# Optimization experiments

Hardware: AMD Instinct MI355X
Metric: run time of the kernel (lower is better)

The kernel has to match this reference:

```python
import jax, jax.numpy as jnp
import numpy as np

N, E, D, H = 20000, 320000, 300, 2
NEG_SLOPE = 0.2  # PyG GATConv default LeakyReLU slope


def setup_inputs() -> dict:
    key = jax.random.key(0)
    ks = jax.random.split(key, 8)
    return {
        "x": jax.random.normal(ks[0], (N, D), dtype=jnp.float32),
        "edge_index": jax.random.randint(ks[1], (2, E), 0, N, dtype=jnp.int64),
        "W": jax.random.normal(ks[2], (D, H, D), dtype=jnp.float32) * 0.05,
        "att_src": jax.random.normal(ks[3], (H, D), dtype=jnp.float32) * 0.05,
        "att_dst": jax.random.normal(ks[4], (H, D), dtype=jnp.float32) * 0.05,
        "bias": jax.random.normal(ks[5], (D,), dtype=jnp.float32) * 0.05,
        "lin_w": jax.random.normal(ks[6], (D, 1), dtype=jnp.float32) * 0.05,
        "lin_b": jax.random.normal(ks[7], (1,), dtype=jnp.float32) * 0.05,
    }


def reference(x, edge_index, W, att_src, att_dst, bias, lin_w, lin_b):
    n = x.shape[0]
    # add self-loops (PyG GATConv default)
    loops = jnp.arange(n, dtype=edge_index.dtype)
    src = jnp.concatenate([edge_index[0], loops])  # [E+N]
    dst = jnp.concatenate([edge_index[1], loops])
    # per-head linear projection: [N, H, D]
    xp = jnp.einsum('nd,dhe->nhe', x, W)
    # per-node attention logits [N, H]
    a_src = jnp.sum(xp * att_src, axis=-1)
    a_dst = jnp.sum(xp * att_dst, axis=-1)
    # per-edge score, LeakyReLU, segment softmax over incoming edges of dst
    e = jax.nn.leaky_relu(a_src[src] + a_dst[dst], NEG_SLOPE)  # [Et, H]
    emax = jax.ops.segment_max(e, dst, num_segments=n)  # self-loops ensure non-empty
    ee = jnp.exp(e - emax[dst])
    denom = jax.ops.segment_sum(ee, dst, num_segments=n)
    alpha = ee / denom[dst]  # [Et, H]
    # weighted scatter-add aggregation
    msg = xp[src] * alpha[:, :, None]  # [Et, H, D]
    out = jax.ops.segment_sum(msg, dst, num_segments=n)  # [N, H, D]
    out = out.mean(axis=1) + bias  # concat=False -> head average, then bias
    out = jax.nn.relu(out)
    return out @ lin_w + lin_b  # [N, 1]
```

## Files before the change

### kernel.cpp

```cpp
#include <hip/hip_runtime.h>
#include <math.h>

#define Nn 20000
#define Ee 320000
#define Dd 300
#define Hh 2
#define Cc 600
#define KP 320
#define MP 20096
#define NP 640
#define SQ 640

typedef _Float16 f16;
typedef __attribute__((ext_vector_type(8))) _Float16 f16x8;
typedef __attribute__((ext_vector_type(4))) _Float16 f16x4;
typedef __attribute__((ext_vector_type(2))) _Float16 f16x2;
typedef __attribute__((ext_vector_type(4))) float f32x4;

__device__ __forceinline__ float lrelu(float x) { return x > 0.f ? x : 0.2f * x; }

__global__ __launch_bounds__(256) void k_cvtX(const float* __restrict__ x, f16* __restrict__ xh) {
  int idx = blockIdx.x * 256 + threadIdx.x;
  const int KQ = KP / 4;
  if (idx >= MP * KQ) return;
  int r = idx / KQ, k0 = (idx - r * KQ) * 4;
  float a0 = 0.f, a1 = 0.f, a2 = 0.f, a3 = 0.f;
  if (r < Nn && k0 < Dd) {
    float4 v = *(const float4*)(x + (size_t)r * Dd + k0);
    a0 = v.x; a1 = v.y; a2 = v.z; a3 = v.w;
  }
  f16x4 h;
  h[0] = (f16)a0; h[1] = (f16)a1; h[2] = (f16)a2; h[3] = (f16)a3;
  *(f16x4*)(xh + (size_t)r * KP + k0) = h;
}

__global__ __launch_bounds__(256) void k_cvtW(const float* __restrict__ W, f16* __restrict__ Wh) {
  int idx = blockIdx.x * 256 + threadIdx.x;
  const int KQ = KP / 4;
  if (idx >= NP * KQ) return;
  int c = idx % NP, k0 = (idx / NP) * 4;
  f16x4 h;
#pragma unroll
  for (int j = 0; j < 4; ++j) {
    int k = k0 + j;
    h[j] = (f16)((k < Dd && c < Cc) ? W[(size_t)k * Cc + c] : 0.f);
  }
  *(f16x4*)(Wh + (size_t)c * KP + k0) = h;
}

__global__ __launch_bounds__(256) void k_prep(const float* __restrict__ W,
                                              const float* __restrict__ att_src,
                                              const float* __restrict__ att_dst,
                                              float* __restrict__ vatt) {
  int wid = (blockIdx.x * 256 + threadIdx.x) >> 6;
  int ln = threadIdx.x & 63;
  if (wid >= Dd) return;
  float s0 = 0.f, s1 = 0.f, t0 = 0.f, t1 = 0.f;
  for (int e = ln; e < Dd; e += 64) {
    float w0 = W[(size_t)wid * Cc + e];
    float w1 = W[(size_t)wid * Cc + Dd + e];
    s0 += w0 * att_src[e];  s1 += w1 * att_src[Dd + e];
    t0 += w0 * att_dst[e];  t1 += w1 * att_dst[Dd + e];
  }
  for (int o = 32; o > 0; o >>= 1) {
    s0 += __shfl_down(s0, o, 64); s1 += __shfl_down(s1, o, 64);
    t0 += __shfl_down(t0, o, 64); t1 += __shfl_down(t1, o, 64);
  }
  if (ln == 0) {
    vatt[wid * 4 + 0] = s0; vatt[wid * 4 + 1] = s1;
    vatt[wid * 4 + 2] = t0; vatt[wid * 4 + 3] = t1;
  }
}

__global__ __launch_bounds__(256) void k_logits2(const float* __restrict__ x,
                                                 const float* __restrict__ vatt,
                                                 float* __restrict__ a_src,
                                                 float* __restrict__ a_dst) {
  int wid = (blockIdx.x * 256 + threadIdx.x) >> 6;
  int ln = threadIdx.x & 63;
  if (wid >= Nn) return;
  const float* xr = x + (size_t)wid * Dd;
  float s0 = 0.f, s1 = 0.f, t0 = 0.f, t1 = 0.f;
  for (int d = ln; d < Dd; d += 64) {
    float xv = xr[d];
    float4 vv = *(const float4*)(vatt + d * 4);
    s0 += xv * vv.x; s1 += xv * vv.y; t0 += xv * vv.z; t1 += xv * vv.w;
  }
  for (int o = 32; o > 0; o >>= 1) {
    s0 += __shfl_down(s0, o, 64); s1 += __shfl_down(s1, o, 64);
    t0 += __shfl_down(t0, o, 64); t1 += __shfl_down(t1, o, 64);
  }
  if (ln == 0) {
    a_src[wid * 2 + 0] = s0; a_src[wid * 2 + 1] = s1;
    a_dst[wid * 2 + 0] = t0; a_dst[wid * 2 + 1] = t1;
  }
}

__global__ __launch_bounds__(256) void k_mm(const f16* __restrict__ xh, const f16* __restrict__ Wh,
                                            f16* __restrict__ xq) {
  __shared__ __align__(16) f16 Ash[128][40];
  __shared__ __align__(16) f16 Bsh[64][40];
  int m0 = blockIdx.x * 128, n0 = blockIdx.y * 64;
  int tid = threadIdx.x, wv = tid >> 6, lane = tid & 63;
  int srow = tid >> 2, skq = (tid & 3) * 8;
  int akq = (lane >> 4) * 8;
  f32x4 acc[2][4] = {};
  for (int ks = 0; ks < KP / 32; ++ks) {
    f16x8 va0 = *(const f16x8*)(xh + (size_t)(m0 + srow) * KP + ks * 32 + skq);
    f16x8 va1 = *(const f16x8*)(xh + (size_t)(m0 + 64 + srow) * KP + ks * 32 + skq);
    f16x8 vb  = *(const f16x8*)(Wh + (size_t)(n0 + srow) * KP + ks * 32 + skq);
    __syncthreads();
    *(f16x8*)&Ash[srow][skq]      = va0;
    *(f16x8*)&Ash[64 + srow][skq] = va1;
    *(f16x8*)&Bsh[srow][skq]      = vb;
    __syncthreads();
    f16x8 fa0 = *(const f16x8*)&Ash[32 * wv + (lane & 15)][akq];
    f16x8 fa1 = *(const f16x8*)&Ash[32 * wv + 16 + (lane & 15)][akq];
#pragma unroll
    for (int nt = 0; nt < 4; ++nt) {
      f16x8 fb = *(const f16x8*)&Bsh[16 * nt + (lane & 15)][akq];
      acc[0][nt] = __builtin_amdgcn_mfma_f32_16x16x32_f16(fa0, fb, acc[0][nt], 0, 0, 0);
      acc[1][nt] = __builtin_amdgcn_mfma_f32_16x16x32_f16(fa1, fb, acc[1][nt], 0, 0, 0);
    }
  }
#pragma unroll
  for (int g = 0; g < 2; ++g) {
#pragma unroll
    for (int nt = 0; nt < 4; ++nt) {
      int col = n0 + 16 * nt + (lane & 15);
      if (col < Cc) {
        int rbase = m0 + 32 * wv + 16 * g + ((lane >> 4) * 4);
#pragma unroll
        for (int i = 0; i < 4; ++i) {
          int row = rbase + i;
          if (row < Nn) xq[(size_t)row * SQ + col] = (f16)acc[g][nt][i];
        }
      }
    }
  }
}

__global__ void k_hist(const int* __restrict__ ei, int* __restrict__ cnt) {
  int e = blockIdx.x * 256 + threadIdx.x;
  if (e < Ee) atomicAdd(&cnt[ei[Ee + e]], 1);
}

__global__ __launch_bounds__(1024) void k_scan(const int* __restrict__ cnt, int* __restrict__ offs) {
  __shared__ int wsum[16];
  __shared__ int carry_s;
  int tid = threadIdx.x, wv = tid >> 6, ln = tid & 63;
  if (tid == 0) carry_s = 0;
  __syncthreads();
  for (int base = 0; base < Nn; base += 1024) {
    int i = base + tid;
    int v = (i < Nn) ? cnt[i] : 0;
    int s = v;
    for (int o = 1; o < 64; o <<= 1) {
      int t = __shfl_up(s, o, 64);
      if (ln >= o) s += t;
    }
    if (ln == 63) wsum[wv] = s;
    __syncthreads();
    if (wv == 0) {
      int w = (ln < 16) ? wsum[ln] : 0;
      for (int o = 1; o < 16; o <<= 1) {
        int t = __shfl_up(w, o, 64);
        if (ln >= o) w += t;
      }
      if (ln < 16) wsum[ln] = w;
    }
    __syncthreads();
    int carry = carry_s;
    int excl = carry + (wv > 0 ? wsum[wv - 1] : 0) + s - v;
    if (i < Nn) offs[i] = excl;
    __syncthreads();
    if (tid == 1023) carry_s = carry + wsum[15];
    __syncthreads();
  }
  if (tid == 0) offs[Nn] = carry_s;
}

__global__ void k_scatter(const int* __restrict__ ei, const int* __restrict__ offs,
                          int* __restrict__ cur, int* __restrict__ srt) {
  int e = blockIdx.x * 256 + threadIdx.x;
  if (e < Ee) {
    int s = ei[e], d = ei[Ee + e];
    int pos = offs[d] + atomicAdd(&cur[d], 1);
    srt[pos] = s;
  }
}

__global__ __launch_bounds__(256) void k_agg(const f16* __restrict__ xq,
    const float* __restrict__ a_src, const float* __restrict__ a_dst,
    const int* __restrict__ offs, const int* __restrict__ srt,
    const float* __restrict__ bias, const float* __restrict__ lin_w,
    const float* __restrict__ lin_b, float* __restrict__ out) {
  __shared__ float sAgg[4][600];
  int tid = threadIdx.x, wv = tid >> 6, ln = tid & 63;
  int n = blockIdx.x * 4 + wv;
  int beg = offs[n], deg = offs[n + 1] - beg;
  float2 adv = *(const float2*)(a_dst + 2 * n);
  float2 asv = *(const float2*)(a_src + 2 * n);
  float se0 = lrelu(asv.x + adv.x), se1 = lrelu(asv.y + adv.y);

  float m0 = se0, m1 = se1, s0 = 0.f, s1 = 0.f;
  int ss = -1; float ee0 = 0.f, ee1 = 0.f;
  for (int base = 0; base < deg; base += 64) {
    if (ln < deg - base) {
      int s = srt[beg + base + ln];
      float2 av = *(const float2*)(a_src + 2 * s);
      ss = s; ee0 = lrelu(av.x + adv.x); ee1 = lrelu(av.y + adv.y);
      if (ee0 > m0) { s0 *= __expf(m0 - ee0); m0 = ee0; }
      s0 += __expf(ee0 - m0);
      if (ee1 > m1) { s1 *= __expf(m1 - ee1); m1 = ee1; }
      s1 += __expf(ee1 - m1);
    }
  }
  for (int o = 32; o > 0; o >>= 1) {
    float om = __shfl_xor(m0, o, 64), os = __shfl_xor(s0, o, 64);
    float nm = fmaxf(m0, om);
    s0 = s0 * __expf(m0 - nm) + os * __expf(om - nm); m0 = nm;
    om = __shfl_xor(m1, o, 64); os = __shfl_xor(s1, o, 64);
    nm = fmaxf(m1, om);
    s1 = s1 * __expf(m1 - nm) + os * __expf(om - nm); m1 = nm;
  }
  { float nm = fmaxf(m0, se0); s0 = s0 * __expf(m0 - nm) + __expf(se0 - nm); m0 = nm; }
  { float nm = fmaxf(m1, se1); s1 = s1 * __expf(m1 - nm) + __expf(se1 - nm); m1 = nm; }
  float inv0 = 1.f / s0, inv1 = 1.f / s1;

  float acc[10] = {};
  auto addrow = [&](const f16* row, float p0, float p1) {
#pragma unroll
    for (int k = 0; k < 5; ++k) {
      int c = 2 * ln + 128 * k;
      if (c < Cc) {
        f16x2 hv = *(const f16x2*)(row + c);
        float p = (c < Dd) ? p0 : p1;
        acc[2 * k]     += p * (float)hv[0];
        acc[2 * k + 1] += p * (float)hv[1];
      }
    }
  };

  if (deg <= 64) {
    float p0 = __expf(ee0 - m0) * inv0, p1 = __expf(ee1 - m1) * inv1;
    for (int j = 0; j < deg; ++j) {
      int s = __shfl(ss, j, 64);
      float q0 = __shfl(p0, j, 64), q1 = __shfl(p1, j, 64);
      addrow(xq + (size_t)s * SQ, q0, q1);
    }
  } else {
    for (int base = 0; base < deg; base += 64) {
      int cnt = min(64, deg - base);
      float p0 = 0.f, p1 = 0.f; int s2 = -1;
      if (ln < cnt) {
        int s = srt[beg + base + ln];
        float2 av = *(const float2*)(a_src + 2 * s);
        s2 = s;
        p0 = __expf(lrelu(av.x + adv.x) - m0) * inv0;
        p1 = __expf(lrelu(av.y + adv.y) - m1) * inv1;
      }
      for (int j = 0; j < cnt; ++j) {
        int s = __shfl(s2, j, 64);
        float q0 = __shfl(p0, j, 64), q1 = __shfl(p1, j, 64);
        addrow(xq + (size_t)s * SQ, q0, q1);
      }
    }
  }
  addrow(xq + (size_t)n * SQ, __expf(se0 - m0) * inv0, __expf(se1 - m1) * inv1);

#pragma unroll
  for (int k = 0; k < 5; ++k) {
    int c = 2 * ln + 128 * k;
    if (c < Cc) { sAgg[wv][c] = acc[2 * k]; sAgg[wv][c + 1] = acc[2 * k + 1]; }
  }
  __syncthreads();

  float part = 0.f;
#pragma unroll
  for (int k = 0; k < 5; ++k) {
    int d = ln + 64 * k;
    if (d < Dd) {
      float v = 0.5f * (sAgg[wv][d] + sAgg[wv][d + Dd]) + bias[d];
      v = fmaxf(v, 0.f);
      part += v * lin_w[d];
    }
  }
  for (int o = 32; o > 0; o >>= 1) part += __shfl_xor(part, o, 64);
  if (ln == 0) out[n] = part + lin_b[0];
}

extern "C" void kernel_launch(void* const* d_in, const int* in_sizes, int n_in,
                              void* d_out, int out_size, void* d_ws, size_t ws_size,
                              hipStream_t stream) {
  const float* x       = (const float*)d_in[0];
  const int*   ei      = (const int*)d_in[1];
  const float* W       = (const float*)d_in[2];
  const float* att_src = (const float*)d_in[3];
  const float* att_dst = (const float*)d_in[4];
  const float* bias    = (const float*)d_in[5];
  const float* lin_w   = (const float*)d_in[6];
  const float* lin_b   = (const float*)d_in[7];
  float* out = (float*)d_out;

  char* ws = (char*)d_ws;
  size_t off = 0;
  auto alloc = [&](size_t bytes) {
    void* p = ws + off;
    off = (off + bytes + 255) & ~(size_t)255;
    return p;
  };
  f16*   xq    = (f16*)alloc((size_t)Nn * SQ * 2);
  f16*   xh    = (f16*)alloc((size_t)MP * KP * 2);
  f16*   Wh    = (f16*)alloc((size_t)NP * KP * 2);
  float* vatt  = (float*)alloc((size_t)Dd * 4 * 4);
  float* a_src = (float*)alloc((size_t)Nn * Hh * 4);
  float* a_dst = (float*)alloc((size_t)Nn * Hh * 4);
  int*   cnt   = (int*)alloc((size_t)Nn * 4);
  int*   offs  = (int*)alloc((size_t)(Nn + 1) * 4);
  int*   cur   = (int*)alloc((size_t)Nn * 4);
  int*   srt   = (int*)alloc((size_t)Ee * 4);

  hipMemsetAsync(cnt, 0, (size_t)Nn * 4, stream);
  hipMemsetAsync(cur, 0, (size_t)Nn * 4, stream);

  k_cvtX<<<(MP * (KP / 4) + 255) / 256, 256, 0, stream>>>(x, xh);
  k_cvtW<<<(NP * (KP / 4) + 255) / 256, 256, 0, stream>>>(W, Wh);
  k_prep<<<(Dd * 64 + 255) / 256, 256, 0, stream>>>(W, att_src, att_dst, vatt);
  k_logits2<<<(Nn * 64 + 255) / 256, 256, 0, stream>>>(x, vatt, a_src, a_dst);
  k_mm<<<dim3(MP / 128, NP / 64), 256, 0, stream>>>(xh, Wh, xq);
  k_hist<<<(Ee + 255) / 256, 256, 0, stream>>>(ei, cnt);
  k_scan<<<1, 1024, 0, stream>>>(cnt, offs);
  k_scatter<<<(Ee + 255) / 256, 256, 0, stream>>>(ei, offs, cur, srt);
  k_agg<<<Nn / 4, 256, 0, stream>>>(xq, a_src, a_dst, offs, srt, bias, lin_w, lin_b, out);
}
```

Baseline: 243.7 us.

## Fuse preprocessing kernels, drop memsets, single-pass scan, widen aggregation loads

```diff
diff --git a/kernel.cpp b/kernel.cpp
--- a/kernel.cpp
+++ b/kernel.cpp
@@ -14,85 +14,80 @@
 typedef _Float16 f16;
 typedef __attribute__((ext_vector_type(8))) _Float16 f16x8;
 typedef __attribute__((ext_vector_type(4))) _Float16 f16x4;
-typedef __attribute__((ext_vector_type(2))) _Float16 f16x2;
 typedef __attribute__((ext_vector_type(4))) float f32x4;
 
 __device__ __forceinline__ float lrelu(float x) { return x > 0.f ? x : 0.2f * x; }
 
-__global__ __launch_bounds__(256) void k_cvtX(const float* __restrict__ x, f16* __restrict__ xh) {
-  int idx = blockIdx.x * 256 + threadIdx.x;
-  const int KQ = KP / 4;
-  if (idx >= MP * KQ) return;
-  int r = idx / KQ, k0 = (idx - r * KQ) * 4;
-  float a0 = 0.f, a1 = 0.f, a2 = 0.f, a3 = 0.f;
-  if (r < Nn && k0 < Dd) {
-    float4 v = *(const float4*)(x + (size_t)r * Dd + k0);
-    a0 = v.x; a1 = v.y; a2 = v.z; a3 = v.w;
-  }
-  f16x4 h;
-  h[0] = (f16)a0; h[1] = (f16)a1; h[2] = (f16)a2; h[3] = (f16)a3;
-  *(f16x4*)(xh + (size_t)r * KP + k0) = h;
-}
-
-__global__ __launch_bounds__(256) void k_cvtW(const float* __restrict__ W, f16* __restrict__ Wh) {
-  int idx = blockIdx.x * 256 + threadIdx.x;
-  const int KQ = KP / 4;
-  if (idx >= NP * KQ) return;
-  int c = idx % NP, k0 = (idx / NP) * 4;
-  f16x4 h;
-#pragma unroll
-  for (int j = 0; j < 4; ++j) {
-    int k = k0 + j;
-    h[j] = (f16)((k < Dd && c < Cc) ? W[(size_t)k * Cc + c] : 0.f);
-  }
-  *(f16x4*)(Wh + (size_t)c * KP + k0) = h;
-}
-
-__global__ __launch_bounds__(256) void k_prep(const float* __restrict__ W,
+__global__ __launch_bounds__(256) void k_pre2(const float* __restrict__ W,
                                               const float* __restrict__ att_src,
                                               const float* __restrict__ att_dst,
-                                              float* __restrict__ vatt) {
-  int wid = (blockIdx.x * 256 + threadIdx.x) >> 6;
-  int ln = threadIdx.x & 63;
-  if (wid >= Dd) return;
+                                              f16* __restrict__ Wh, float* __restrict__ vatt) {
+  int idx = blockIdx.x * 256 + threadIdx.x;
+  {
+    int c = idx % NP, k0 = (idx / NP) * 4;
+    f16x4 h;
+#pragma unroll
+    for (int j = 0; j < 4; ++j) {
+      int k = k0 + j;
+      h[j] = (f16)((k < Dd && c < Cc) ? W[(size_t)k * Cc + c] : 0.f);
+    }
+    *(f16x4*)(Wh + (size_t)c * KP + k0) = h;
+  }
+  int wid = idx >> 6, ln = idx & 63;
+  if (wid < Dd) {
+    float s0 = 0.f, s1 = 0.f, t0 = 0.f, t1 = 0.f;
+    for (int e = ln; e < Dd; e += 64) {
+      float w0 = W[(size_t)wid * Cc + e];
+      float w1 = W[(size_t)wid * Cc + Dd + e];
+      s0 += w0 * att_src[e];  s1 += w1 * att_src[Dd + e];
+      t0 += w0 * att_dst[e];  t1 += w1 * att_dst[Dd + e];
+    }
+    for (int o = 32; o > 0; o >>= 1) {
+      s0 += __shfl_down(s0, o, 64); s1 += __shfl_down(s1, o, 64);
+      t0 += __shfl_down(t0, o, 64); t1 += __shfl_down(t1, o, 64);
+    }
+    if (ln == 0) {
+      vatt[wid * 4 + 0] = s0; vatt[wid * 4 + 1] = s1;
+      vatt[wid * 4 + 2] = t0; vatt[wid * 4 + 3] = t1;
+    }
+  }
+}
+
+__global__ __launch_bounds__(256) void k_pre1(const float* __restrict__ x,
+                                              const float* __restrict__ vatt,
+                                              f16* __restrict__ xh,
+                                              float* __restrict__ a_src, float* __restrict__ a_dst,
+                                              int* __restrict__ cnt) {
+  int gid = blockIdx.x * 256 + threadIdx.x;
+  if (gid < Nn) cnt[gid] = 0;
+  int wv = threadIdx.x >> 6, ln = threadIdx.x & 63;
+  int n = blockIdx.x * 4 + wv;
+  if (n >= MP) return;
+  if (n >= Nn) {
+#pragma unroll
+    for (int k = 0; k < 5; ++k) xh[(size_t)n * KP + ln + 64 * k] = (f16)0.f;
+    return;
+  }
+  const float* xr = x + (size_t)n * Dd;
   float s0 = 0.f, s1 = 0.f, t0 = 0.f, t1 = 0.f;
-  for (int e = ln; e < Dd; e += 64) {
-    float w0 = W[(size_t)wid * Cc + e];
-    float w1 = W[(size_t)wid * Cc + Dd + e];
-    s0 += w0 * att_src[e];  s1 += w1 * att_src[Dd + e];
-    t0 += w0 * att_dst[e];  t1 += w1 * att_dst[Dd + e];
+#pragma unroll
+  for (int k = 0; k < 5; ++k) {
+    int d = ln + 64 * k;
+    float xv = 0.f;
+    if (d < Dd) {
+      xv = xr[d];
+      float4 vv = *(const float4*)(vatt + d * 4);
+      s0 += xv * vv.x; s1 += xv * vv.y; t0 += xv * vv.z; t1 += xv * vv.w;
+    }
+    xh[(size_t)n * KP + d] = (f16)xv;
   }
   for (int o = 32; o > 0; o >>= 1) {
     s0 += __shfl_down(s0, o, 64); s1 += __shfl_down(s1, o, 64);
     t0 += __shfl_down(t0, o, 64); t1 += __shfl_down(t1, o, 64);
   }
   if (ln == 0) {
-    vatt[wid * 4 + 0] = s0; vatt[wid * 4 + 1] = s1;
-    vatt[wid * 4 + 2] = t0; vatt[wid * 4 + 3] = t1;
-  }
-}
-
-__global__ __launch_bounds__(256) void k_logits2(const float* __restrict__ x,
-                                                 const float* __restrict__ vatt,
-                                                 float* __restrict__ a_src,
-                                                 float* __restrict__ a_dst) {
-  int wid = (blockIdx.x * 256 + threadIdx.x) >> 6;
-  int ln = threadIdx.x & 63;
-  if (wid >= Nn) return;
-  const float* xr = x + (size_t)wid * Dd;
-  float s0 = 0.f, s1 = 0.f, t0 = 0.f, t1 = 0.f;
-  for (int d = ln; d < Dd; d += 64) {
-    float xv = xr[d];
-    float4 vv = *(const float4*)(vatt + d * 4);
-    s0 += xv * vv.x; s1 += xv * vv.y; t0 += xv * vv.z; t1 += xv * vv.w;
-  }
-  for (int o = 32; o > 0; o >>= 1) {
-    s0 += __shfl_down(s0, o, 64); s1 += __shfl_down(s1, o, 64);
-    t0 += __shfl_down(t0, o, 64); t1 += __shfl_down(t1, o, 64);
-  }
-  if (ln == 0) {
-    a_src[wid * 2 + 0] = s0; a_src[wid * 2 + 1] = s1;
-    a_dst[wid * 2 + 0] = t0; a_dst[wid * 2 + 1] = t1;
+    a_src[n * 2 + 0] = s0; a_src[n * 2 + 1] = s1;
+    a_dst[n * 2 + 0] = t0; a_dst[n * 2 + 1] = t1;
   }
 }
 
@@ -145,47 +140,57 @@
   if (e < Ee) atomicAdd(&cnt[ei[Ee + e]], 1);
 }
 
-__global__ __launch_bounds__(1024) void k_scan(const int* __restrict__ cnt, int* __restrict__ offs) {
+__global__ __launch_bounds__(1024) void k_scan(const int* __restrict__ cnt,
+                                               int* __restrict__ offs, int* __restrict__ cur) {
   __shared__ int wsum[16];
-  __shared__ int carry_s;
-  int tid = threadIdx.x, wv = tid >> 6, ln = tid & 63;
-  if (tid == 0) carry_s = 0;
+  int t = threadIdx.x, wv = t >> 6, ln = t & 63;
+  int i0 = t * 20;
+  int v[20];
+  int tot = 0;
+  if (i0 < Nn) {
+    const int4* p = (const int4*)(cnt + i0);
+#pragma unroll
+    for (int q = 0; q < 5; ++q) {
+      int4 w = p[q];
+      v[4 * q] = w.x; v[4 * q + 1] = w.y; v[4 * q + 2] = w.z; v[4 * q + 3] = w.w;
+    }
+#pragma unroll
+    for (int j = 0; j < 20; ++j) tot += v[j];
+  }
+  int s = tot;
+  for (int o = 1; o < 64; o <<= 1) {
+    int u = __shfl_up(s, o, 64);
+    if (ln >= o) s += u;
+  }
+  if (ln == 63) wsum[wv] = s;
   __syncthreads();
-  for (int base = 0; base < Nn; base += 1024) {
-    int i = base + tid;
-    int v = (i < Nn) ? cnt[i] : 0;
-    int s = v;
-    for (int o = 1; o < 64; o <<= 1) {
-      int t = __shfl_up(s, o, 64);
-      if (ln >= o) s += t;
-    }
-    if (ln == 63) wsum[wv] = s;
-    __syncthreads();
-    if (wv == 0) {
-      int w = (ln < 16) ? wsum[ln] : 0;
-      for (int o = 1; o < 16; o <<= 1) {
-        int t = __shfl_up(w, o, 64);
-        if (ln >= o) w += t;
-      }
-      if (ln < 16) wsum[ln] = w;
-    }
-    __syncthreads();
-    int carry = carry_s;
-    int excl = carry + (wv > 0 ? wsum[wv - 1] : 0) + s - v;
-    if (i < Nn) offs[i] = excl;
-    __syncthreads();
-    if (tid == 1023) carry_s = carry + wsum[15];
-    __syncthreads();
-  }
-  if (tid == 0) offs[Nn] = carry_s;
-}
-
-__global__ void k_scatter(const int* __restrict__ ei, const int* __restrict__ offs,
-                          int* __restrict__ cur, int* __restrict__ srt) {
+  if (wv == 0) {
+    int w = (ln < 16) ? wsum[ln] : 0;
+    for (int o = 1; o < 16; o <<= 1) {
+      int u = __shfl_up(w, o, 64);
+      if (ln >= o) w += u;
+    }
+    if (ln < 16) wsum[ln] = w;
+  }
+  __syncthreads();
+  if (i0 < Nn) {
+    int run = (wv > 0 ? wsum[wv - 1] : 0) + (s - tot);
+#pragma unroll
+    for (int j = 0; j < 20; ++j) {
+      offs[i0 + j] = run;
+      cur[i0 + j] = run;
+      run += v[j];
+    }
+  }
+  if (t == 0) offs[Nn] = wsum[15];
+}
+
+__global__ void k_scatter(const int* __restrict__ ei, int* __restrict__ cur,
+                          int* __restrict__ srt) {
   int e = blockIdx.x * 256 + threadIdx.x;
   if (e < Ee) {
     int s = ei[e], d = ei[Ee + e];
-    int pos = offs[d] + atomicAdd(&cur[d], 1);
+    int pos = atomicAdd(&cur[d], 1);
     srt[pos] = s;
   }
 }
@@ -228,22 +233,25 @@
   { float nm = fmaxf(m1, se1); s1 = s1 * __expf(m1 - nm) + __expf(se1 - nm); m1 = nm; }
   float inv0 = 1.f / s0, inv1 = 1.f / s1;
 
-  float acc[10] = {};
+  float acc[12] = {};
   auto addrow = [&](const f16* row, float p0, float p1) {
 #pragma unroll
-    for (int k = 0; k < 5; ++k) {
-      int c = 2 * ln + 128 * k;
+    for (int k = 0; k < 3; ++k) {
+      int c = 4 * ln + 256 * k;
       if (c < Cc) {
-        f16x2 hv = *(const f16x2*)(row + c);
+        f16x4 hv = *(const f16x4*)(row + c);
         float p = (c < Dd) ? p0 : p1;
-        acc[2 * k]     += p * (float)hv[0];
-        acc[2 * k + 1] += p * (float)hv[1];
+        acc[4 * k + 0] += p * (float)hv[0];
+        acc[4 * k + 1] += p * (float)hv[1];
+        acc[4 * k + 2] += p * (float)hv[2];
+        acc[4 * k + 3] += p * (float)hv[3];
       }
     }
   };
 
   if (deg <= 64) {
     float p0 = __expf(ee0 - m0) * inv0, p1 = __expf(ee1 - m1) * inv1;
+#pragma unroll 2
     for (int j = 0; j < deg; ++j) {
       int s = __shfl(ss, j, 64);
       float q0 = __shfl(p0, j, 64), q1 = __shfl(p1, j, 64);
@@ -251,16 +259,17 @@
     }
   } else {
     for (int base = 0; base < deg; base += 64) {
-      int cnt = min(64, deg - base);
+      int cnt2 = min(64, deg - base);
       float p0 = 0.f, p1 = 0.f; int s2 = -1;
-      if (ln < cnt) {
+      if (ln < cnt2) {
         int s = srt[beg + base + ln];
         float2 av = *(const float2*)(a_src + 2 * s);
         s2 = s;
         p0 = __expf(lrelu(av.x + adv.x) - m0) * inv0;
         p1 = __expf(lrelu(av.y + adv.y) - m1) * inv1;
       }
-      for (int j = 0; j < cnt; ++j) {
+#pragma unroll 2
+      for (int j = 0; j < cnt2; ++j) {
         int s = __shfl(s2, j, 64);
         float q0 = __shfl(p0, j, 64), q1 = __shfl(p1, j, 64);
         addrow(xq + (size_t)s * SQ, q0, q1);
@@ -270,9 +279,12 @@
   addrow(xq + (size_t)n * SQ, __expf(se0 - m0) * inv0, __expf(se1 - m1) * inv1);
 
 #pragma unroll
-  for (int k = 0; k < 5; ++k) {
-    int c = 2 * ln + 128 * k;
-    if (c < Cc) { sAgg[wv][c] = acc[2 * k]; sAgg[wv][c + 1] = acc[2 * k + 1]; }
+  for (int k = 0; k < 3; ++k) {
+    int c = 4 * ln + 256 * k;
+    if (c < Cc) {
+#pragma unroll
+      for (int j = 0; j < 4; ++j) sAgg[wv][c + j] = acc[4 * k + j];
+    }
   }
   __syncthreads();
 
@@ -321,16 +333,11 @@
   int*   cur   = (int*)alloc((size_t)Nn * 4);
   int*   srt   = (int*)alloc((size_t)Ee * 4);
 
-  hipMemsetAsync(cnt, 0, (size_t)Nn * 4, stream);
-  hipMemsetAsync(cur, 0, (size_t)Nn * 4, stream);
-
-  k_cvtX<<<(MP * (KP / 4) + 255) / 256, 256, 0, stream>>>(x, xh);
-  k_cvtW<<<(NP * (KP / 4) + 255) / 256, 256, 0, stream>>>(W, Wh);
-  k_prep<<<(Dd * 64 + 255) / 256, 256, 0, stream>>>(W, att_src, att_dst, vatt);
-  k_logits2<<<(Nn * 64 + 255) / 256, 256, 0, stream>>>(x, vatt, a_src, a_dst);
+  k_pre2<<<NP * (KP / 4) / 256, 256, 0, stream>>>(W, att_src, att_dst, Wh, vatt);
+  k_pre1<<<MP / 4, 256, 0, stream>>>(x, vatt, xh, a_src, a_dst, cnt);
   k_mm<<<dim3(MP / 128, NP / 64), 256, 0, stream>>>(xh, Wh, xq);
   k_hist<<<(Ee + 255) / 256, 256, 0, stream>>>(ei, cnt);
-  k_scan<<<1, 1024, 0, stream>>>(cnt, offs);
-  k_scatter<<<(Ee + 255) / 256, 256, 0, stream>>>(ei, offs, cur, srt);
+  k_scan<<<1, 1024, 0, stream>>>(cnt, offs, cur);
+  k_scatter<<<(Ee + 255) / 256, 256, 0, stream>>>(ei, cur, srt);
   k_agg<<<Nn / 4, 256, 0, stream>>>(xq, a_src, a_dst, offs, srt, bias, lin_w, lin_b, out);
 }
```

Result: faster. 221.2 us (-9.2%).
